# Performance work log

Hardware: AMD Instinct MI355X
Metric: run time of the kernel (lower is better)

The kernel has to match this reference:

```python
import jax, jax.numpy as jnp
import numpy as np

N, E, F_IN, EDGE_DIM = 50000, 1600000, 128, 16
H, C = 4, 32            # heads, per-head channels for conv1/conv2
C_OUT = 2               # conv3: heads=1, out_channels=2
HC = H * C              # 128 = hidden_channels * heads
NEG_SLOPE = 0.2
BN_EPS = 1e-5


def setup_inputs() -> dict:
    key = jax.random.key(0)
    ks = jax.random.split(key, 40)
    rn = lambda k, s, sc: jax.random.normal(k, s, jnp.float32) * sc
    inp = {}
    inp["x"] = rn(ks[0], (N, F_IN), 1.0)
    inp["edge_index"] = jax.random.randint(ks[1], (2, E), 0, N, dtype=jnp.int32)
    inp["edge_attr"] = rn(ks[2], (E, EDGE_DIM), 1.0)
    # GATConv layer 1 (in=F_IN -> H x C)
    inp["W1"] = rn(ks[3], (F_IN, HC), F_IN ** -0.5)
    inp["as1"] = rn(ks[4], (H, C), 0.1)
    inp["ad1"] = rn(ks[5], (H, C), 0.1)
    inp["We1"] = rn(ks[6], (EDGE_DIM, HC), EDGE_DIM ** -0.5)
    inp["ae1"] = rn(ks[7], (H, C), 0.1)
    inp["b1"] = jnp.zeros((HC,), jnp.float32)
    # BN1 (eval mode: running stats)
    inp["g1"] = jnp.ones((HC,), jnp.float32)
    inp["be1"] = jnp.zeros((HC,), jnp.float32)
    inp["rm1"] = rn(ks[8], (HC,), 0.1)
    inp["rv1"] = jnp.ones((HC,), jnp.float32)
    # GATConv layer 2 (in=HC -> H x C)
    inp["W2"] = rn(ks[9], (HC, HC), HC ** -0.5)
    inp["as2"] = rn(ks[10], (H, C), 0.1)
    inp["ad2"] = rn(ks[11], (H, C), 0.1)
    inp["We2"] = rn(ks[12], (EDGE_DIM, HC), EDGE_DIM ** -0.5)
    inp["ae2"] = rn(ks[13], (H, C), 0.1)
    inp["b2"] = jnp.zeros((HC,), jnp.float32)
    inp["g2"] = jnp.ones((HC,), jnp.float32)
    inp["be2"] = jnp.zeros((HC,), jnp.float32)
    inp["rm2"] = rn(ks[14], (HC,), 0.1)
    inp["rv2"] = jnp.ones((HC,), jnp.float32)
    inp["W3"] = rn(ks[15], (HC, C_OUT), HC ** -0.5)
    inp["as3"] = rn(ks[16], (1, C_OUT), 0.1)
    inp["ad3"] = rn(ks[17], (1, C_OUT), 0.1)
    inp["We3"] = rn(ks[18], (EDGE_DIM, C_OUT), EDGE_DIM ** -0.5)
    inp["ae3"] = rn(ks[19], (1, C_OUT), 0.1)
    inp["b3"] = jnp.zeros((C_OUT,), jnp.float32)
    return inp


def _gat_layer(x, src, dst, eattr, W, a_s, a_d, We, a_e, b, heads, ch):
    """PyG GATConv (shared src/dst linear, edge_dim, add_self_loops already applied)."""
    n = x.shape[0]
    xp = (x @ W).reshape(n, heads, ch)                      # [N,H,C]
    alpha_src = (xp * a_s).sum(-1)                          # [N,H]
    alpha_dst = (xp * a_d).sum(-1)                          # [N,H]
    ep = (eattr @ We).reshape(-1, heads, ch)                # [E,H,C]
    alpha_e = (ep * a_e).sum(-1)                            # [E,H]
    alpha = alpha_src[src] + alpha_dst[dst] + alpha_e       # [E,H]
    alpha = jax.nn.leaky_relu(alpha, NEG_SLOPE)
    # segment softmax over incoming edges of each dst node
    m = jax.ops.segment_max(alpha, dst, num_segments=n)     # every node has a self loop
    ex = jnp.exp(alpha - m[dst])
    s = jax.ops.segment_sum(ex, dst, num_segments=n)
    alpha = ex / (s[dst] + 1e-16)                           # [E,H]
    msg = xp[src] * alpha[..., None]                        # [E,H,C]
    out = jax.ops.segment_sum(msg, dst, num_segments=n)     # [N,H,C]
    return out.reshape(n, heads * ch) + b


def _bn_eval(x, g, b, rm, rv):
    return (x - rm) * (g * jax.lax.rsqrt(rv + BN_EPS)) + b


def reference(x, edge_index, edge_attr,
              W1, as1, ad1, We1, ae1, b1, g1, be1, rm1, rv1,
              W2, as2, ad2, We2, ae2, b2, g2, be2, rm2, rv2,
              W3, as3, ad3, We3, ae3, b3):
    n = x.shape[0]
    loop = jnp.arange(n, dtype=edge_index.dtype)
    src = jnp.concatenate([edge_index[0], loop])
    dst = jnp.concatenate([edge_index[1], loop])
    # self-loop edge_attr fill_value='mean' (PyG default)
    ea_mean = jnp.broadcast_to(edge_attr.mean(0), (n, edge_attr.shape[1]))
    ea = jnp.concatenate([edge_attr, ea_mean], axis=0)

    h = _gat_layer(x, src, dst, ea, W1, as1, ad1, We1, ae1, b1, H, C)
    h = jax.nn.elu(_bn_eval(h, g1, be1, rm1, rv1))
    h = _gat_layer(h, src, dst, ea, W2, as2, ad2, We2, ae2, b2, H, C)
    h = jax.nn.elu(_bn_eval(h, g2, be2, rm2, rv2))
    out = _gat_layer(h, src, dst, ea, W3, as3, ad3, We3, ae3, b3, 1, C_OUT)
    return out
```

## Files before the change

### kernel.cpp

```cpp
#include <hip/hip_runtime.h>
#include <hip/hip_fp16.h>
#include <math.h>

#define NN 50000
#define EE 1600000
#define ETOT (EE + NN)
#define NEG_SLOPE 0.2f
#define BN_EPS 1e-5f
#define PAY_BLOCKS 1024
#define NB_SCAN ((NN + 255) / 256)
#define NPB 128
#define NBUCK ((NN + NPB - 1) / NPB)
#define CHUNK 8192
#define NCHUNK ((EE + CHUNK - 1) / CHUNK)


static __device__ inline unsigned pkh2(float a, float b) {
  __half ha = __float2half_rn(a), hb = __float2half_rn(b);
  unsigned short ua = *(unsigned short*)&ha, ub = *(unsigned short*)&hb;
  return ((unsigned)ub << 16) | ua;
}
static __device__ inline float upkh(unsigned u, int hi) {
  unsigned short s = hi ? (unsigned short)(u >> 16) : (unsigned short)(u & 0xffff);
  __half h = *(__half*)&s;
  return __half2float(h);
}

__global__ void compute_M_k(const float* __restrict__ We1, const float* __restrict__ ae1,
                            const float* __restrict__ We2, const float* __restrict__ ae2,
                            const float* __restrict__ We3, const float* __restrict__ ae3,
                            float* __restrict__ M) {
  int t = threadIdx.x;
  if (t < 64) {
    int d = t >> 2, h = t & 3;
    float s1 = 0.f, s2 = 0.f;
    for (int c = 0; c < 32; ++c) {
      s1 += We1[d * 128 + h * 32 + c] * ae1[h * 32 + c];
      s2 += We2[d * 128 + h * 32 + c] * ae2[h * 32 + c];
    }
    M[t] = s1;
    M[64 + t] = s2;
  }
  if (t < 16) {
    M[128 + t] = We3[t * 2] * ae3[0] + We3[t * 2 + 1] * ae3[1];
  }
}

__global__ __launch_bounds__(256) void payload_k(const int* __restrict__ src,
                                                 const int* __restrict__ dst,
                                                 const float* __restrict__ ea,
                                                 const float* __restrict__ M,
                                                 int* __restrict__ deg,
                                                 float4* __restrict__ payload,
                                                 float* __restrict__ mean_part) {
  __shared__ float sM[144];
  int t = threadIdx.x;
  if (t < 144) sM[t] = M[t];
  __syncthreads();
  float macc[16];
#pragma unroll
  for (int d = 0; d < 16; ++d) macc[d] = 0.f;

  for (int e = blockIdx.x * 256 + t; e < EE; e += PAY_BLOCKS * 256) {
    float v[16];
    const float4* p = (const float4*)(ea + (size_t)e * 16);
    float4 q0 = p[0], q1 = p[1], q2 = p[2], q3 = p[3];
    v[0] = q0.x; v[1] = q0.y; v[2] = q0.z; v[3] = q0.w;
    v[4] = q1.x; v[5] = q1.y; v[6] = q1.z; v[7] = q1.w;
    v[8] = q2.x; v[9] = q2.y; v[10] = q2.z; v[11] = q2.w;
    v[12] = q3.x; v[13] = q3.y; v[14] = q3.z; v[15] = q3.w;
    float a1[4], a2[4];
#pragma unroll
    for (int h = 0; h < 4; ++h) {
      float s1 = 0.f, s2 = 0.f;
#pragma unroll
      for (int d = 0; d < 16; ++d) {
        s1 += v[d] * sM[d * 4 + h];
        s2 += v[d] * sM[64 + d * 4 + h];
      }
      a1[h] = s1; a2[h] = s2;
    }
    float a3 = 0.f;
#pragma unroll
    for (int d = 0; d < 16; ++d) a3 += v[d] * sM[128 + d];
#pragma unroll
    for (int d = 0; d < 16; ++d) macc[d] += v[d];

    atomicAdd(&deg[dst[e]], 1);
    float4 r0, r1;
    r0.x = __uint_as_float(pkh2(a1[0], a1[1]));
    r0.y = __uint_as_float(pkh2(a1[2], a1[3]));
    r0.z = __uint_as_float(pkh2(a2[0], a2[1]));
    r0.w = __uint_as_float(pkh2(a2[2], a2[3]));
    r1.x = a3;
    r1.y = __int_as_float(src[e]);
    r1.z = 0.f; r1.w = 0.f;
    payload[(size_t)e * 2] = r0;
    payload[(size_t)e * 2 + 1] = r1;
  }
#pragma unroll
  for (int d = 0; d < 16; ++d) {
#pragma unroll
    for (int off = 32; off; off >>= 1) macc[d] += __shfl_xor(macc[d], off, 64);
  }
  __shared__ float swsum[4][16];
  int w = t >> 6, l = t & 63;
  if (l == 0) {
#pragma unroll
    for (int d = 0; d < 16; ++d) swsum[w][d] = macc[d];
  }
  __syncthreads();
  if (t < 16) {
    mean_part[(size_t)blockIdx.x * 16 + t] =
        swsum[0][t] + swsum[1][t] + swsum[2][t] + swsum[3][t];
  }
}

__global__ __launch_bounds__(256) void selfloop_k(const float* __restrict__ mean_part,
                                                  const float* __restrict__ M,
                                                  float* __restrict__ alpha_sl) {
  __shared__ float s[256];
  int t = threadIdx.x;
  int d = t & 15, c = t >> 4;
  float v = 0.f;
  for (int i = c * 64; i < (c + 1) * 64; ++i) v += mean_part[(size_t)i * 16 + d];
  s[t] = v;
  __syncthreads();
  if (t < 16) {
    float sum = 0.f;
    for (int c2 = 0; c2 < 16; ++c2) sum += s[c2 * 16 + t];
    s[t] = sum / (float)EE;
  }
  __syncthreads();
  if (t < 9) {
    float r = 0.f;
    if (t < 4) {
      for (int dd = 0; dd < 16; ++dd) r += s[dd] * M[dd * 4 + t];
    } else if (t < 8) {
      int h = t - 4;
      for (int dd = 0; dd < 16; ++dd) r += s[dd] * M[64 + dd * 4 + h];
    } else {
      for (int dd = 0; dd < 16; ++dd) r += s[dd] * M[128 + dd];
    }
    alpha_sl[t] = r;
  }
}

__global__ __launch_bounds__(256) void scan_part_k(const int* __restrict__ deg,
                                                   int* __restrict__ part) {
  int t = threadIdx.x;
  int i = blockIdx.x * 256 + t;
  int v = (i < NN) ? deg[i] + 1 : 0;
#pragma unroll
  for (int off = 32; off; off >>= 1) v += __shfl_xor(v, off, 64);
  __shared__ int s[4];
  if ((t & 63) == 0) s[t >> 6] = v;
  __syncthreads();
  if (t == 0) part[blockIdx.x] = s[0] + s[1] + s[2] + s[3];
}

__global__ __launch_bounds__(256) void scan_base_k(int* __restrict__ part) {
  __shared__ int s[256];
  int t = threadIdx.x;
  int v = (t < NB_SCAN) ? part[t] : 0;
  s[t] = v;
  __syncthreads();
  for (int off = 1; off < 256; off <<= 1) {
    int u = (t >= off) ? s[t - off] : 0;
    __syncthreads();
    s[t] += u;
    __syncthreads();
  }
  if (t < NB_SCAN) part[t] = s[t] - v;
}

__global__ __launch_bounds__(256) void scan_fill_k(const int* __restrict__ deg,
                                                   const int* __restrict__ part,
                                                   int* __restrict__ row_ofs) {
  __shared__ int s[256];
  int t = threadIdx.x;
  int i = blockIdx.x * 256 + t;
  int v = (i < NN) ? deg[i] + 1 : 0;
  s[t] = v;
  __syncthreads();
  for (int off = 1; off < 256; off <<= 1) {
    int u = (t >= off) ? s[t - off] : 0;
    __syncthreads();
    s[t] += u;
    __syncthreads();
  }
  int excl = s[t] - v + part[blockIdx.x];
  if (i < NN) row_ofs[i] = excl;
  if (i == NN - 1) row_ofs[NN] = ETOT;
}

__global__ void binit_k(const int* __restrict__ row_ofs, int* __restrict__ bcur) {
  int b = blockIdx.x * blockDim.x + threadIdx.x;
  if (b < NBUCK) bcur[b] = row_ofs[b * NPB] - b * NPB;
}

__global__ __launch_bounds__(256) void bscat_k(const int* __restrict__ dst,
                                               int* __restrict__ bcur,
                                               unsigned* __restrict__ pairs) {
  __shared__ int hist[512];
  __shared__ int ofs[512];
  int t = threadIdx.x;
  for (int c = blockIdx.x; c < NCHUNK; c += gridDim.x) {
    int cb = c * CHUNK;
    for (int b = t; b < 512; b += 256) hist[b] = 0;
    __syncthreads();
#pragma unroll
    for (int k = 0; k < 8; ++k) {
      int e = cb + k * 1024 + t * 4;
      if (e < EE) {
        int4 d4 = *(const int4*)&dst[e];
        atomicAdd(&hist[d4.x >> 7], 1);
        atomicAdd(&hist[d4.y >> 7], 1);
        atomicAdd(&hist[d4.z >> 7], 1);
        atomicAdd(&hist[d4.w >> 7], 1);
      }
    }
    __syncthreads();
    for (int b = t; b < NBUCK; b += 256) {
      int h = hist[b];
      ofs[b] = h ? atomicAdd(&bcur[b], h) : 0;
      hist[b] = 0;
    }
    __syncthreads();
#pragma unroll
    for (int k = 0; k < 8; ++k) {
      int e = cb + k * 1024 + t * 4;
      if (e < EE) {
        int4 d4 = *(const int4*)&dst[e];
        int dd[4] = {d4.x, d4.y, d4.z, d4.w};
#pragma unroll
        for (int j = 0; j < 4; ++j) {
          int b = dd[j] >> 7;
          int pos = ofs[b] + atomicAdd(&hist[b], 1);
          pairs[pos] = ((unsigned)(dd[j] & (NPB - 1)) << 21) | (unsigned)(e + j);
        }
      }
    }
    __syncthreads();
  }
}

__global__ __launch_bounds__(256) void cbuild_k(const int* __restrict__ row_ofs,
                                                const unsigned* __restrict__ pairs,
                                                const float4* __restrict__ payload,
                                                const float* __restrict__ asl,
                                                uint2* __restrict__ recAE1,
                                                uint2* __restrict__ recAE2,
                                                float* __restrict__ rec3,
                                                int* __restrict__ recSrc) {
  __shared__ int cur[NPB];
  int b = blockIdx.x;
  int t = threadIdx.x;
  int n0 = b * NPB;
  int n1 = n0 + NPB; if (n1 > NN) n1 = NN;
  int nn = n1 - n0;
  uint2 a1s = make_uint2(pkh2(asl[0], asl[1]), pkh2(asl[2], asl[3]));
  uint2 a2s = make_uint2(pkh2(asl[4], asl[5]), pkh2(asl[6], asl[7]));
  float a3s = asl[8];
  if (t < nn) {
    int p = row_ofs[n0 + t];
    cur[t] = p + 1;
    recAE1[p] = a1s; recAE2[p] = a2s; rec3[p] = a3s; recSrc[p] = n0 + t;
  }
  __syncthreads();
  int pb = row_ofs[n0] - n0;
  int pe = row_ofs[n1] - n1;
  for (int i0 = pb + t; i0 < pe; i0 += 1024) {
    unsigned u[4];
    bool valid[4];
    float4 p0[4], p1[4];
    int pos[4];
#pragma unroll
    for (int k = 0; k < 4; ++k) {
      int i = i0 + k * 256;
      valid[k] = (i < pe);
      if (valid[k]) u[k] = pairs[i];
    }
#pragma unroll
    for (int k = 0; k < 4; ++k) {
      if (valid[k]) {
        int eid = u[k] & 0x1FFFFF;
        p0[k] = payload[(size_t)eid * 2];
        p1[k] = payload[(size_t)eid * 2 + 1];
        pos[k] = atomicAdd(&cur[u[k] >> 21], 1);
      }
    }
#pragma unroll
    for (int k = 0; k < 4; ++k) {
      if (valid[k]) {
        recAE1[pos[k]] = make_uint2(__float_as_uint(p0[k].x), __float_as_uint(p0[k].y));
        recAE2[pos[k]] = make_uint2(__float_as_uint(p0[k].z), __float_as_uint(p0[k].w));
        rec3[pos[k]] = p1[k].x;
        recSrc[pos[k]] = __float_as_int(p1[k].y);
      }
    }
  }
}

__global__ __launch_bounds__(256) void gemm128a_k(const float* __restrict__ X,
                                                  const float* __restrict__ W,
                                                  const float* __restrict__ as,
                                                  const float* __restrict__ ad,
                                                  __half* __restrict__ Y,
                                                  float* __restrict__ asrc,
                                                  float* __restrict__ adst,
                                                  int nrows) {
  __shared__ float sW[128 * 64];
  __shared__ float sX[64 * 132];
  __shared__ float sas[128], sad[128];
  int t = threadIdx.x;
  int r0 = blockIdx.x * 64;
  int cb = blockIdx.y;
  if (t < 128) { sas[t] = as[t]; sad[t] = ad[t]; }
#pragma unroll
  for (int i = 0; i < 8; ++i) {
    int flat = t + i * 256;
    int k = flat >> 4, c4 = flat & 15;
    *(float4*)&sW[k * 64 + c4 * 4] = *(const float4*)&W[k * 128 + cb * 64 + c4 * 4];
  }
  int rows = nrows - r0; if (rows > 64) rows = 64;
#pragma unroll
  for (int i = 0; i < 8; ++i) {
    int flat = t + i * 256;
    int r = flat >> 5, k4 = flat & 31;
    if (r < rows)
      *(float4*)&sX[r * 132 + k4 * 4] = *(const float4*)&X[(size_t)(r0 + r) * 128 + k4 * 4];
  }
  __syncthreads();
  int cq = t & 15, rl = t >> 4;
  float4 acc[4];
#pragma unroll
  for (int i = 0; i < 4; ++i) acc[i] = make_float4(0.f, 0.f, 0.f, 0.f);

  for (int k = 0; k < 128; k += 4) {
    float4 w0 = *(float4*)&sW[(k + 0) * 64 + cq * 4];
    float4 w1 = *(float4*)&sW[(k + 1) * 64 + cq * 4];
    float4 w2 = *(float4*)&sW[(k + 2) * 64 + cq * 4];
    float4 w3 = *(float4*)&sW[(k + 3) * 64 + cq * 4];
#pragma unroll
    for (int i = 0; i < 4; ++i) {
      float4 xv = *(float4*)&sX[(rl + i * 16) * 132 + k];
      acc[i].x += xv.x * w0.x + xv.y * w1.x + xv.z * w2.x + xv.w * w3.x;
      acc[i].y += xv.x * w0.y + xv.y * w1.y + xv.z * w2.y + xv.w * w3.y;
      acc[i].z += xv.x * w0.z + xv.y * w1.z + xv.z * w2.z + xv.w * w3.z;
      acc[i].w += xv.x * w0.w + xv.y * w1.w + xv.z * w2.w + xv.w * w3.w;
    }
  }
  int h = cb * 2 + (cq >> 3);
  int col0 = cb * 64 + cq * 4;
#pragma unroll
  for (int i = 0; i < 4; ++i) {
    int r = rl + i * 16;
    if (r < rows) {
      uint2 st;
      st.x = pkh2(acc[i].x, acc[i].y);
      st.y = pkh2(acc[i].z, acc[i].w);
      *(uint2*)&Y[(size_t)(r0 + r) * 128 + col0] = st;
      float s1 = acc[i].x * sas[col0] + acc[i].y * sas[col0 + 1] +
                 acc[i].z * sas[col0 + 2] + acc[i].w * sas[col0 + 3];
      float s2 = acc[i].x * sad[col0] + acc[i].y * sad[col0 + 1] +
                 acc[i].z * sad[col0 + 2] + acc[i].w * sad[col0 + 3];
      s1 += __shfl_xor(s1, 1, 8); s1 += __shfl_xor(s1, 2, 8); s1 += __shfl_xor(s1, 4, 8);
      s2 += __shfl_xor(s2, 1, 8); s2 += __shfl_xor(s2, 2, 8); s2 += __shfl_xor(s2, 4, 8);
      if ((cq & 7) == 0) {
        asrc[(size_t)(r0 + r) * 4 + h] = s1;
        adst[(size_t)(r0 + r) * 4 + h] = s2;
      }
    }
  }
}

__global__ __launch_bounds__(128) void agg128_k(
    const int* __restrict__ row_ofs, const unsigned* __restrict__ recAE,
    const int* __restrict__ recSrc, const __half* __restrict__ xp,
    const float* __restrict__ asrc, const float* __restrict__ adst,
    const float* __restrict__ bias, const float* __restrict__ g,
    const float* __restrict__ be, const float* __restrict__ rm,
    const float* __restrict__ rv, float* __restrict__ out) {
  int n = blockIdx.x;
  int t = threadIdx.x;
  int h = t >> 5, j = t & 31;
  int e4 = t >> 4, gg = t & 15;
  int hh = gg >> 2;
  __shared__ float s_w[4 * 64];
  __shared__ int s_src[64];
  __shared__ float sf[4], sden[4];
  __shared__ float sacc[8][132];
  int beg = row_ofs[n], end = row_ofs[n + 1];
  float adn = adst[(size_t)n * 4 + h];
  float m_run = -1e30f, s_run = 0.f;
  float acc[8];
#pragma unroll
  for (int i = 0; i < 8; ++i) acc[i] = 0.f;

  for (int base = beg; base < end; base += 64) {
    int cnt = end - base; if (cnt > 64) cnt = 64;
    float a0 = -1e30f, a1 = -1e30f;
    if (j < cnt) {
      int idx = base + j;
      float ae = upkh(recAE[(size_t)idx * 2 + (h >> 1)], h & 1);
      int sj = recSrc[idx];
      if (h == 0) s_src[j] = sj;
      float a = asrc[(size_t)sj * 4 + h] + adn + ae;
      a0 = (a > 0.f) ? a : NEG_SLOPE * a;
    }
    if (j + 32 < cnt) {
      int idx = base + j + 32;
      float ae = upkh(recAE[(size_t)idx * 2 + (h >> 1)], h & 1);
      int sj = recSrc[idx];
      if (h == 0) s_src[j + 32] = sj;
      float a = asrc[(size_t)sj * 4 + h] + adn + ae;
      a1 = (a > 0.f) ? a : NEG_SLOPE * a;
    }
    float cm = fmaxf(a0, a1);
#pragma unroll
    for (int off = 16; off; off >>= 1) cm = fmaxf(cm, __shfl_xor(cm, off, 32));
    float f = 1.f;
    if (cm > m_run) { f = expf(m_run - cm); s_run *= f; m_run = cm; }
    if (j == 0) sf[h] = f;
    float ex0 = (j < cnt) ? expf(a0 - m_run) : 0.f;
    float ex1 = (j + 32 < cnt) ? expf(a1 - m_run) : 0.f;
    s_w[h * 64 + j] = ex0;
    s_w[h * 64 + j + 32] = ex1;
    float se = ex0 + ex1;
#pragma unroll
    for (int off = 16; off; off >>= 1) se += __shfl_xor(se, off, 32);
    s_run += se;
    __syncthreads();
    float ff = sf[hh];
    if (ff != 1.f) {
#pragma unroll
      for (int i = 0; i < 8; ++i) acc[i] *= ff;
    }
    for (int e2 = 0; e2 < cnt; e2 += 16) {
      int ed0 = e2 + e4, ed1 = e2 + e4 + 8;
      bool b0 = ed0 < cnt, b1 = ed1 < cnt;
      uint4 v0, v1;
      float w0 = 0.f, w1 = 0.f;
      if (b0) {
        int s0 = s_src[ed0]; w0 = s_w[hh * 64 + ed0];
        v0 = *(const uint4*)&xp[(size_t)s0 * 128 + gg * 8];
      }
      if (b1) {
        int s1 = s_src[ed1]; w1 = s_w[hh * 64 + ed1];
        v1 = *(const uint4*)&xp[(size_t)s1 * 128 + gg * 8];
      }
      if (b0) {
        acc[0] += w0 * upkh(v0.x, 0); acc[1] += w0 * upkh(v0.x, 1);
        acc[2] += w0 * upkh(v0.y, 0); acc[3] += w0 * upkh(v0.y, 1);
        acc[4] += w0 * upkh(v0.z, 0); acc[5] += w0 * upkh(v0.z, 1);
        acc[6] += w0 * upkh(v0.w, 0); acc[7] += w0 * upkh(v0.w, 1);
      }
      if (b1) {
        acc[0] += w1 * upkh(v1.x, 0); acc[1] += w1 * upkh(v1.x, 1);
        acc[2] += w1 * upkh(v1.y, 0); acc[3] += w1 * upkh(v1.y, 1);
        acc[4] += w1 * upkh(v1.z, 0); acc[5] += w1 * upkh(v1.z, 1);
        acc[6] += w1 * upkh(v1.w, 0); acc[7] += w1 * upkh(v1.w, 1);
      }
    }
    __syncthreads();
  }
  if (j == 0) sden[h] = s_run;
#pragma unroll
  for (int i = 0; i < 8; ++i) sacc[e4][gg * 8 + i] = acc[i];
  __syncthreads();
  float v = 0.f;
#pragma unroll
  for (int i = 0; i < 8; ++i) v += sacc[i][t];
  v = v / (sden[t >> 5] + 1e-16f) + bias[t];
  v = (v - rm[t]) * (g[t] * rsqrtf(rv[t] + BN_EPS)) + be[t];
  v = (v > 0.f) ? v : (expf(v) - 1.f);
  out[(size_t)n * 128 + t] = v;
}

__global__ __launch_bounds__(256) void xp3_k(const float* __restrict__ h2,
                                             const float* __restrict__ W3,
                                             const float* __restrict__ as3,
                                             const float* __restrict__ ad3,
                                             float* __restrict__ xp3,
                                             float* __restrict__ asrc3,
                                             float* __restrict__ adst3) {
  __shared__ float sW[256];
  int t = threadIdx.x;
  sW[t] = W3[t];
  __syncthreads();
  int n = blockIdx.x * 256 + t;
  if (n < NN) {
    const float4* row = (const float4*)(h2 + (size_t)n * 128);
    float y0 = 0.f, y1 = 0.f;
#pragma unroll
    for (int i = 0; i < 32; ++i) {
      float4 v = row[i];
      y0 += v.x * sW[(i * 4 + 0) * 2] + v.y * sW[(i * 4 + 1) * 2] +
            v.z * sW[(i * 4 + 2) * 2] + v.w * sW[(i * 4 + 3) * 2];
      y1 += v.x * sW[(i * 4 + 0) * 2 + 1] + v.y * sW[(i * 4 + 1) * 2 + 1] +
            v.z * sW[(i * 4 + 2) * 2 + 1] + v.w * sW[(i * 4 + 3) * 2 + 1];
    }
    xp3[n * 2] = y0;
    xp3[n * 2 + 1] = y1;
    asrc3[n] = y0 * as3[0] + y1 * as3[1];
    adst3[n] = y0 * ad3[0] + y1 * ad3[1];
  }
}

__global__ __launch_bounds__(256) void agg2_k(const int* __restrict__ row_ofs,
                                              const float* __restrict__ rec3,
                                              const int* __restrict__ recSrc,
                                              const float* __restrict__ xp3,
                                              const float* __restrict__ asrc3,
                                              const float* __restrict__ adst3,
                                              const float* __restrict__ b3,
                                              float* __restrict__ out) {
  int t = threadIdx.x;
  int w = t >> 6, l = t & 63;
  int n = blockIdx.x * 4 + w;
  if (n >= NN) return;
  int beg = row_ofs[n], end = row_ofs[n + 1];
  float adn = adst3[n];
  float m = -1e30f, s = 0.f, a0 = 0.f, a1 = 0.f;
  for (int idx = beg + l; idx < end; idx += 64) {
    float aev = rec3[idx];
    int sj = recSrc[idx];
    float a = asrc3[sj] + adn + aev;
    a = (a > 0.f) ? a : NEG_SLOPE * a;
    if (a > m) {
      float f = expf(m - a);
      s *= f; a0 *= f; a1 *= f; m = a;
    }
    float ex = expf(a - m);
    s += ex;
    a0 += ex * xp3[sj * 2];
    a1 += ex * xp3[sj * 2 + 1];
  }
  float M = m;
#pragma unroll
  for (int off = 32; off; off >>= 1) M = fmaxf(M, __shfl_xor(M, off, 64));
  float f = expf(m - M);
  s *= f; a0 *= f; a1 *= f;
#pragma unroll
  for (int off = 32; off; off >>= 1) {
    s += __shfl_xor(s, off, 64);
    a0 += __shfl_xor(a0, off, 64);
    a1 += __shfl_xor(a1, off, 64);
  }
  if (l == 0) {
    float inv = 1.f / (s + 1e-16f);
    out[n * 2] = a0 * inv + b3[0];
    out[n * 2 + 1] = a1 * inv + b3[1];
  }
}

extern "C" void kernel_launch(void* const* d_in, const int* in_sizes, int n_in,
                              void* d_out, int out_size, void* d_ws, size_t ws_size,
                              hipStream_t stream) {
  const float* x   = (const float*)d_in[0];
  const int*   ei  = (const int*)d_in[1];
  const float* ea  = (const float*)d_in[2];
  const float* W1  = (const float*)d_in[3];
  const float* as1 = (const float*)d_in[4];
  const float* ad1 = (const float*)d_in[5];
  const float* We1 = (const float*)d_in[6];
  const float* ae1 = (const float*)d_in[7];
  const float* b1  = (const float*)d_in[8];
  const float* g1  = (const float*)d_in[9];
  const float* be1 = (const float*)d_in[10];
  const float* rm1 = (const float*)d_in[11];
  const float* rv1 = (const float*)d_in[12];
  const float* W2  = (const float*)d_in[13];
  const float* as2 = (const float*)d_in[14];
  const float* ad2 = (const float*)d_in[15];
  const float* We2 = (const float*)d_in[16];
  const float* ae2 = (const float*)d_in[17];
  const float* b2  = (const float*)d_in[18];
  const float* g2  = (const float*)d_in[19];
  const float* be2 = (const float*)d_in[20];
  const float* rm2 = (const float*)d_in[21];
  const float* rv2 = (const float*)d_in[22];
  const float* W3  = (const float*)d_in[23];
  const float* as3 = (const float*)d_in[24];
  const float* ad3 = (const float*)d_in[25];
  const float* We3 = (const float*)d_in[26];
  const float* ae3 = (const float*)d_in[27];
  const float* b3  = (const float*)d_in[28];

  const int* srcA = ei;
  const int* dstA = ei + EE;

  char* p = (char*)d_ws;
  auto alloc = [&](size_t bytes) -> void* {
    void* r = (void*)p;
    p += (bytes + 255) & ~(size_t)255;
    return r;
  };
  float4* payload = (float4*)alloc(32 * (size_t)EE);
  uint2* recAE1 = (uint2*)alloc(sizeof(uint2) * (size_t)ETOT);
  uint2* recAE2 = (uint2*)alloc(sizeof(uint2) * (size_t)ETOT);
  float* rec3   = (float*)alloc(sizeof(float) * (size_t)ETOT);
  int*   recSrc = (int*)alloc(sizeof(int) * (size_t)ETOT);
  unsigned* pairs = (unsigned*)alloc(sizeof(unsigned) * (size_t)EE);
  __half* xp    = (__half*)alloc(sizeof(__half) * (size_t)NN * 128);
  float* hbuf   = (float*)alloc(sizeof(float) * (size_t)NN * 128);
  float* Mbuf   = (float*)alloc(sizeof(float) * 144);
  float* meanp  = (float*)alloc(sizeof(float) * (size_t)PAY_BLOCKS * 16);
  float* asl    = (float*)alloc(sizeof(float) * 12);
  float* asrc   = (float*)alloc(sizeof(float) * (size_t)NN * 4);
  float* adst   = (float*)alloc(sizeof(float) * (size_t)NN * 4);
  float* xp3    = (float*)alloc(sizeof(float) * (size_t)NN * 2);
  float* asrc3  = (float*)alloc(sizeof(float) * (size_t)NN);
  float* adst3  = (float*)alloc(sizeof(float) * (size_t)NN);
  int* deg      = (int*)alloc(sizeof(int) * (size_t)NN);
  int* part     = (int*)alloc(sizeof(int) * 256);
  int* row_ofs  = (int*)alloc(sizeof(int) * (size_t)(NN + 1));
  int* bcur     = (int*)alloc(sizeof(int) * (size_t)NBUCK);

  hipMemsetAsync(deg, 0, NN * sizeof(int), stream);

  compute_M_k<<<1, 64, 0, stream>>>(We1, ae1, We2, ae2, We3, ae3, Mbuf);
  payload_k<<<PAY_BLOCKS, 256, 0, stream>>>(srcA, dstA, ea, Mbuf, deg, payload, meanp);
  selfloop_k<<<1, 256, 0, stream>>>(meanp, Mbuf, asl);
  scan_part_k<<<NB_SCAN, 256, 0, stream>>>(deg, part);
  scan_base_k<<<1, 256, 0, stream>>>(part);
  scan_fill_k<<<NB_SCAN, 256, 0, stream>>>(deg, part, row_ofs);
  binit_k<<<(NBUCK + 255) / 256, 256, 0, stream>>>(row_ofs, bcur);
  bscat_k<<<200, 256, 0, stream>>>(dstA, bcur, pairs);
  cbuild_k<<<NBUCK, 256, 0, stream>>>(row_ofs, pairs, payload, asl,
                                      recAE1, recAE2, rec3, recSrc);

  gemm128a_k<<<dim3((NN + 63) / 64, 2), 256, 0, stream>>>(x, W1, as1, ad1, xp, asrc, adst, NN);
  agg128_k<<<NN, 128, 0, stream>>>(row_ofs, (const unsigned*)recAE1, recSrc, xp,
                                   asrc, adst, b1, g1, be1, rm1, rv1, hbuf);
  gemm128a_k<<<dim3((NN + 63) / 64, 2), 256, 0, stream>>>(hbuf, W2, as2, ad2, xp, asrc, adst, NN);
  agg128_k<<<NN, 128, 0, stream>>>(row_ofs, (const unsigned*)recAE2, recSrc, xp,
                                   asrc, adst, b2, g2, be2, rm2, rv2, hbuf);
  xp3_k<<<(NN + 255) / 256, 256, 0, stream>>>(hbuf, W3, as3, ad3, xp3, asrc3, adst3);
  agg2_k<<<(NN + 3) / 4, 256, 0, stream>>>(row_ofs, rec3, recSrc, xp3, asrc3, adst3,
                                           b3, (float*)d_out);
}
```

Baseline: 432.2 us.

## Replace per-node degree atomics and scan with bucket histogram and in-block CSR offsets

The per-edge global atomicAdd into a degree array and the three-kernel scan over 50K nodes are removed. They are replaced by a shared-memory bucket histogram, a single-block scan over 391 buckets, and per-node offset computation inside cbuild from the bucketed pairs. The edge payload is also shrunk from 32 bytes to 24 bytes, split into separate uint4 and uint2 arrays. This cuts global atomic contention and kernel launches, but adds a shared-memory count pass in cbuild and an extra read of dst.

```diff
diff --git a/kernel.cpp b/kernel.cpp
--- a/kernel.cpp
+++ b/kernel.cpp
@@ -8,7 +8,6 @@
 #define NEG_SLOPE 0.2f
 #define BN_EPS 1e-5f
 #define PAY_BLOCKS 1024
-#define NB_SCAN ((NN + 255) / 256)
 #define NPB 128
 #define NBUCK ((NN + NPB - 1) / NPB)
 #define CHUNK 8192
@@ -47,11 +46,10 @@
 }
 
 __global__ __launch_bounds__(256) void payload_k(const int* __restrict__ src,
-                                                 const int* __restrict__ dst,
                                                  const float* __restrict__ ea,
                                                  const float* __restrict__ M,
-                                                 int* __restrict__ deg,
-                                                 float4* __restrict__ payload,
+                                                 uint4* __restrict__ payA,
+                                                 uint2* __restrict__ payB,
                                                  float* __restrict__ mean_part) {
   __shared__ float sM[144];
   int t = threadIdx.x;
@@ -86,17 +84,9 @@
 #pragma unroll
     for (int d = 0; d < 16; ++d) macc[d] += v[d];
 
-    atomicAdd(&deg[dst[e]], 1);
-    float4 r0, r1;
-    r0.x = __uint_as_float(pkh2(a1[0], a1[1]));
-    r0.y = __uint_as_float(pkh2(a1[2], a1[3]));
-    r0.z = __uint_as_float(pkh2(a2[0], a2[1]));
-    r0.w = __uint_as_float(pkh2(a2[2], a2[3]));
-    r1.x = a3;
-    r1.y = __int_as_float(src[e]);
-    r1.z = 0.f; r1.w = 0.f;
-    payload[(size_t)e * 2] = r0;
-    payload[(size_t)e * 2 + 1] = r1;
+    payA[e] = make_uint4(pkh2(a1[0], a1[1]), pkh2(a1[2], a1[3]),
+                         pkh2(a2[0], a2[1]), pkh2(a2[2], a2[3]));
+    payB[e] = make_uint2(__float_as_uint(a3), (unsigned)src[e]);
   }
 #pragma unroll
   for (int d = 0; d < 16; ++d) {
@@ -146,57 +136,52 @@
   }
 }
 
-__global__ __launch_bounds__(256) void scan_part_k(const int* __restrict__ deg,
-                                                   int* __restrict__ part) {
-  int t = threadIdx.x;
-  int i = blockIdx.x * 256 + t;
-  int v = (i < NN) ? deg[i] + 1 : 0;
-#pragma unroll
-  for (int off = 32; off; off >>= 1) v += __shfl_xor(v, off, 64);
-  __shared__ int s[4];
-  if ((t & 63) == 0) s[t >> 6] = v;
-  __syncthreads();
-  if (t == 0) part[blockIdx.x] = s[0] + s[1] + s[2] + s[3];
-}
-
-__global__ __launch_bounds__(256) void scan_base_k(int* __restrict__ part) {
-  __shared__ int s[256];
-  int t = threadIdx.x;
-  int v = (t < NB_SCAN) ? part[t] : 0;
-  s[t] = v;
-  __syncthreads();
-  for (int off = 1; off < 256; off <<= 1) {
-    int u = (t >= off) ? s[t - off] : 0;
-    __syncthreads();
-    s[t] += u;
-    __syncthreads();
-  }
-  if (t < NB_SCAN) part[t] = s[t] - v;
-}
-
-__global__ __launch_bounds__(256) void scan_fill_k(const int* __restrict__ deg,
-                                                   const int* __restrict__ part,
-                                                   int* __restrict__ row_ofs) {
-  __shared__ int s[256];
-  int t = threadIdx.x;
-  int i = blockIdx.x * 256 + t;
-  int v = (i < NN) ? deg[i] + 1 : 0;
-  s[t] = v;
-  __syncthreads();
-  for (int off = 1; off < 256; off <<= 1) {
-    int u = (t >= off) ? s[t - off] : 0;
-    __syncthreads();
-    s[t] += u;
-    __syncthreads();
-  }
-  int excl = s[t] - v + part[blockIdx.x];
-  if (i < NN) row_ofs[i] = excl;
-  if (i == NN - 1) row_ofs[NN] = ETOT;
-}
-
-__global__ void binit_k(const int* __restrict__ row_ofs, int* __restrict__ bcur) {
-  int b = blockIdx.x * blockDim.x + threadIdx.x;
-  if (b < NBUCK) bcur[b] = row_ofs[b * NPB] - b * NPB;
+__global__ __launch_bounds__(256) void bcount_k(const int* __restrict__ dst,
+                                                int* __restrict__ bucketCnt) {
+  __shared__ int hist[512];
+  int t = threadIdx.x;
+  for (int b = t; b < 512; b += 256) hist[b] = 0;
+  __syncthreads();
+  for (int e = (blockIdx.x * 256 + t) * 4; e < EE; e += gridDim.x * 1024) {
+    int4 d4 = *(const int4*)&dst[e];
+    atomicAdd(&hist[d4.x >> 7], 1);
+    atomicAdd(&hist[d4.y >> 7], 1);
+    atomicAdd(&hist[d4.z >> 7], 1);
+    atomicAdd(&hist[d4.w >> 7], 1);
+  }
+  __syncthreads();
+  for (int b = t; b < NBUCK; b += 256)
+    if (hist[b]) atomicAdd(&bucketCnt[b], hist[b]);
+}
+
+__global__ __launch_bounds__(512) void bscan_k(const int* __restrict__ bucketCnt,
+                                               int* __restrict__ pBase,
+                                               int* __restrict__ rBase,
+                                               int* __restrict__ bcur) {
+  __shared__ int s1[512], s2[512];
+  int t = threadIdx.x;
+  int cnt = (t < NBUCK) ? bucketCnt[t] : 0;
+  int nn = 0;
+  if (t < NBUCK) {
+    int n0 = t * NPB;
+    nn = NN - n0; if (nn > NPB) nn = NPB;
+  }
+  s1[t] = cnt;
+  s2[t] = cnt + nn;
+  __syncthreads();
+  for (int off = 1; off < 512; off <<= 1) {
+    int a = (t >= off) ? s1[t - off] : 0;
+    int b = (t >= off) ? s2[t - off] : 0;
+    __syncthreads();
+    s1[t] += a; s2[t] += b;
+    __syncthreads();
+  }
+  if (t < NBUCK) {
+    pBase[t] = s1[t] - cnt;
+    rBase[t] = s2[t] - (cnt + nn);
+    bcur[t] = s1[t] - cnt;
+  }
+  if (t == 0) { pBase[NBUCK] = EE; rBase[NBUCK] = ETOT; }
 }
 
 __global__ __launch_bounds__(256) void bscat_k(const int* __restrict__ dst,
@@ -245,35 +230,55 @@
   }
 }
 
-__global__ __launch_bounds__(256) void cbuild_k(const int* __restrict__ row_ofs,
+__global__ __launch_bounds__(256) void cbuild_k(const int* __restrict__ pBase,
+                                                const int* __restrict__ rBase,
                                                 const unsigned* __restrict__ pairs,
-                                                const float4* __restrict__ payload,
+                                                const uint4* __restrict__ payA,
+                                                const uint2* __restrict__ payB,
                                                 const float* __restrict__ asl,
                                                 uint2* __restrict__ recAE1,
                                                 uint2* __restrict__ recAE2,
                                                 float* __restrict__ rec3,
-                                                int* __restrict__ recSrc) {
+                                                int* __restrict__ recSrc,
+                                                int* __restrict__ row_ofs) {
+  __shared__ int lcnt[NPB];
+  __shared__ int ss[NPB];
   __shared__ int cur[NPB];
   int b = blockIdx.x;
   int t = threadIdx.x;
   int n0 = b * NPB;
   int n1 = n0 + NPB; if (n1 > NN) n1 = NN;
   int nn = n1 - n0;
+  int pb = pBase[b], pe = pBase[b + 1];
+  if (t < NPB) lcnt[t] = 0;
+  __syncthreads();
+  for (int i = pb + t; i < pe; i += 256) atomicAdd(&lcnt[pairs[i] >> 21], 1);
+  __syncthreads();
+  int v = (t < nn) ? (lcnt[t] + 1) : 0;
+  if (t < NPB) ss[t] = v;
+  __syncthreads();
+  for (int off = 1; off < NPB; off <<= 1) {
+    int a = (t >= off && t < NPB) ? ss[t - off] : 0;
+    __syncthreads();
+    if (t < NPB) ss[t] += a;
+    __syncthreads();
+  }
   uint2 a1s = make_uint2(pkh2(asl[0], asl[1]), pkh2(asl[2], asl[3]));
   uint2 a2s = make_uint2(pkh2(asl[4], asl[5]), pkh2(asl[6], asl[7]));
   float a3s = asl[8];
+  int rb = rBase[b];
   if (t < nn) {
-    int p = row_ofs[n0 + t];
-    cur[t] = p + 1;
-    recAE1[p] = a1s; recAE2[p] = a2s; rec3[p] = a3s; recSrc[p] = n0 + t;
-  }
-  __syncthreads();
-  int pb = row_ofs[n0] - n0;
-  int pe = row_ofs[n1] - n1;
+    int self = rb + ss[t] - v;
+    row_ofs[n0 + t] = self;
+    cur[t] = self + 1;
+    recAE1[self] = a1s; recAE2[self] = a2s; rec3[self] = a3s; recSrc[self] = n0 + t;
+  }
+  if (b == NBUCK - 1 && t == 0) row_ofs[NN] = ETOT;
+  __syncthreads();
   for (int i0 = pb + t; i0 < pe; i0 += 1024) {
     unsigned u[4];
     bool valid[4];
-    float4 p0[4], p1[4];
+    uint4 pA[4]; uint2 pB[4];
     int pos[4];
 #pragma unroll
     for (int k = 0; k < 4; ++k) {
@@ -285,18 +290,18 @@
     for (int k = 0; k < 4; ++k) {
       if (valid[k]) {
         int eid = u[k] & 0x1FFFFF;
-        p0[k] = payload[(size_t)eid * 2];
-        p1[k] = payload[(size_t)eid * 2 + 1];
+        pA[k] = payA[eid];
+        pB[k] = payB[eid];
         pos[k] = atomicAdd(&cur[u[k] >> 21], 1);
       }
     }
 #pragma unroll
     for (int k = 0; k < 4; ++k) {
       if (valid[k]) {
-        recAE1[pos[k]] = make_uint2(__float_as_uint(p0[k].x), __float_as_uint(p0[k].y));
-        recAE2[pos[k]] = make_uint2(__float_as_uint(p0[k].z), __float_as_uint(p0[k].w));
-        rec3[pos[k]] = p1[k].x;
-        recSrc[pos[k]] = __float_as_int(p1[k].y);
+        recAE1[pos[k]] = make_uint2(pA[k].x, pA[k].y);
+        recAE2[pos[k]] = make_uint2(pA[k].z, pA[k].w);
+        rec3[pos[k]] = __uint_as_float(pB[k].x);
+        recSrc[pos[k]] = (int)pB[k].y;
       }
     }
   }
@@ -597,7 +602,8 @@
     p += (bytes + 255) & ~(size_t)255;
     return r;
   };
-  float4* payload = (float4*)alloc(32 * (size_t)EE);
+  uint4* payA   = (uint4*)alloc(sizeof(uint4) * (size_t)EE);
+  uint2* payB   = (uint2*)alloc(sizeof(uint2) * (size_t)EE);
   uint2* recAE1 = (uint2*)alloc(sizeof(uint2) * (size_t)ETOT);
   uint2* recAE2 = (uint2*)alloc(sizeof(uint2) * (size_t)ETOT);
   float* rec3   = (float*)alloc(sizeof(float) * (size_t)ETOT);
@@ -613,23 +619,22 @@
   float* xp3    = (float*)alloc(sizeof(float) * (size_t)NN * 2);
   float* asrc3  = (float*)alloc(sizeof(float) * (size_t)NN);
   float* adst3  = (float*)alloc(sizeof(float) * (size_t)NN);
-  int* deg      = (int*)alloc(sizeof(int) * (size_t)NN);
-  int* part     = (int*)alloc(sizeof(int) * 256);
+  int* bucketCnt = (int*)alloc(sizeof(int) * (size_t)NBUCK);
+  int* pBase    = (int*)alloc(sizeof(int) * (size_t)(NBUCK + 1));
+  int* rBase    = (int*)alloc(sizeof(int) * (size_t)(NBUCK + 1));
+  int* bcur     = (int*)alloc(sizeof(int) * (size_t)NBUCK);
   int* row_ofs  = (int*)alloc(sizeof(int) * (size_t)(NN + 1));
-  int* bcur     = (int*)alloc(sizeof(int) * (size_t)NBUCK);
-
-  hipMemsetAsync(deg, 0, NN * sizeof(int), stream);
+
+  hipMemsetAsync(bucketCnt, 0, NBUCK * sizeof(int), stream);
 
   compute_M_k<<<1, 64, 0, stream>>>(We1, ae1, We2, ae2, We3, ae3, Mbuf);
-  payload_k<<<PAY_BLOCKS, 256, 0, stream>>>(srcA, dstA, ea, Mbuf, deg, payload, meanp);
+  payload_k<<<PAY_BLOCKS, 256, 0, stream>>>(srcA, ea, Mbuf, payA, payB, meanp);
   selfloop_k<<<1, 256, 0, stream>>>(meanp, Mbuf, asl);
-  scan_part_k<<<NB_SCAN, 256, 0, stream>>>(deg, part);
-  scan_base_k<<<1, 256, 0, stream>>>(part);
-  scan_fill_k<<<NB_SCAN, 256, 0, stream>>>(deg, part, row_ofs);
-  binit_k<<<(NBUCK + 255) / 256, 256, 0, stream>>>(row_ofs, bcur);
+  bcount_k<<<256, 256, 0, stream>>>(dstA, bucketCnt);
+  bscan_k<<<1, 512, 0, stream>>>(bucketCnt, pBase, rBase, bcur);
   bscat_k<<<200, 256, 0, stream>>>(dstA, bcur, pairs);
-  cbuild_k<<<NBUCK, 256, 0, stream>>>(row_ofs, pairs, payload, asl,
-                                      recAE1, recAE2, rec3, recSrc);
+  cbuild_k<<<NBUCK, 256, 0, stream>>>(pBase, rBase, pairs, payA, payB, asl,
+                                      recAE1, recAE2, rec3, recSrc, row_ofs);
 
   gemm128a_k<<<dim3((NN + 63) / 64, 2), 256, 0, stream>>>(x, W1, as1, ad1, xp, asrc, adst, NN);
   agg128_k<<<NN, 128, 0, stream>>>(row_ofs, (const unsigned*)recAE1, recSrc, xp,
```

Measured after the change: 409.3 us. 1.06x faster.
